# Kernel optimization log

Hardware: AMD Instinct MI355X
Metric: run time of the kernel (lower is better)

The kernel has to match this reference:

```python
import jax, jax.numpy as jnp
import numpy as np

D_MODEL = 1024
D_STATE = 32
D_CONV = 4
D_INNER = 2 * D_MODEL          # mamba default expand=2
DT_RANK = D_MODEL // 16        # 'auto' -> ceil(d_model/16)
BATCH, SEQ = 4, 2048
LN_EPS = 1e-5


def setup_inputs() -> dict:
    key = jax.random.key(0)
    ks = jax.random.split(key, 8)
    s = 0.02
    # S4D-real init for A_log, as in mamba_ssm
    A_log = jnp.log(jnp.tile(jnp.arange(1, D_STATE + 1, dtype=jnp.float32)[None, :], (D_INNER, 1)))
    return {
        "x": jax.random.normal(ks[0], (BATCH, SEQ, D_MODEL), jnp.float32),
        "in_proj_w": jax.random.normal(ks[1], (D_MODEL, 2 * D_INNER), jnp.float32) * s,
        "conv_w": jax.random.normal(ks[2], (D_INNER, D_CONV), jnp.float32) * s,
        "conv_b": jnp.zeros((D_INNER,), jnp.float32),
        "x_proj_w": jax.random.normal(ks[3], (D_INNER, DT_RANK + 2 * D_STATE), jnp.float32) * s,
        "dt_proj_w": jax.random.normal(ks[4], (DT_RANK, D_INNER), jnp.float32) * s,
        "dt_proj_b": jax.random.uniform(ks[5], (D_INNER,), jnp.float32, -4.0, -2.0),  # softplus -> small dt
        "A_log": A_log,
        "D": jnp.ones((D_INNER,), jnp.float32),
        "out_proj_w": jax.random.normal(ks[6], (D_INNER, D_MODEL), jnp.float32) * s,
        "ln_gamma": jnp.ones((D_MODEL,), jnp.float32),
        "ln_beta": jnp.zeros((D_MODEL,), jnp.float32),
    }


def reference(x, in_proj_w, conv_w, conv_b, x_proj_w, dt_proj_w, dt_proj_b,
              A_log, D, out_proj_w, ln_gamma, ln_beta):
    Bb, Ll, _ = x.shape
    # in_proj -> split into ssm branch (xi) and gate (z)
    xz = x @ in_proj_w                              # [B,L,2*Di]
    xi, z = jnp.split(xz, 2, axis=-1)               # each [B,L,Di]

    # causal depthwise conv1d (kernel D_CONV), left-padded, truncated to L
    xp = jnp.pad(xi, ((0, 0), (D_CONV - 1, 0), (0, 0)))
    xc = conv_b
    for k in range(D_CONV):
        xc = xc + xp[:, k:k + Ll, :] * conv_w[None, None, :, k]
    xi = jax.nn.silu(xc)                            # [B,L,Di]

    # x_proj -> dt, B, C
    dbc = xi @ x_proj_w                             # [B,L,dt_rank+2*S]
    dt = dbc[..., :DT_RANK]
    Bm = dbc[..., DT_RANK:DT_RANK + D_STATE]        # [B,L,S]
    Cm = dbc[..., DT_RANK + D_STATE:]               # [B,L,S]
    delta = jax.nn.softplus(dt @ dt_proj_w + dt_proj_b)  # [B,L,Di]

    A = -jnp.exp(A_log)                             # [Di,S]

    def step(h, inp):
        dl, bt, ct, ut = inp                        # [B,Di],[B,S],[B,S],[B,Di]
        dA = jnp.exp(dl[..., None] * A)             # [B,Di,S]
        h = dA * h + (dl * ut)[..., None] * bt[:, None, :]
        y = jnp.einsum('bds,bs->bd', h, ct)
        return h, y

    h0 = jnp.zeros((Bb, D_INNER, D_STATE), x.dtype)
    xs = (delta.transpose(1, 0, 2), Bm.transpose(1, 0, 2),
          Cm.transpose(1, 0, 2), xi.transpose(1, 0, 2))
    _, ys = jax.lax.scan(step, h0, xs)              # ys: [L,B,Di]

    y = ys.transpose(1, 0, 2) + xi * D              # skip term u*D
    y = y * jax.nn.silu(z)                          # gate
    out = y @ out_proj_w                            # [B,L,d_model]

    # LayerNorm(d_model)
    mu = out.mean(-1, keepdims=True)
    var = out.var(-1, keepdims=True)
    return (out - mu) / jnp.sqrt(var + LN_EPS) * ln_gamma + ln_beta
```

## Files before the change

### kernel.cpp

```cpp
#include <hip/hip_runtime.h>
#include <math.h>

#define D_MODEL 1024
#define D_STATE 32
#define D_CONV  4
#define D_INNER 2048
#define DT_RANK 64
#define BATCH   4
#define SEQ     2048
#define NTOK    (BATCH*SEQ)
#define DBC_N   (DT_RANK + 2*D_STATE)
#define NC      64
#define CL      (SEQ/NC)
#define KSPLIT  8
#define LOG2E   1.4426950408889634f

typedef unsigned short u16;
typedef short bf16x8 __attribute__((ext_vector_type(8)));
typedef float f32x4  __attribute__((ext_vector_type(4)));

__device__ __forceinline__ float bf2f(u16 u){
  return __uint_as_float(((unsigned)u) << 16);
}
__device__ __forceinline__ u16 f2bf(float f){
  unsigned u = __float_as_uint(f);
  return (u16)((u + 0x7fffu + ((u >> 16) & 1u)) >> 16);
}
__device__ __forceinline__ float sigmoidf_(float x){ return 1.f/(1.f+__expf(-x)); }
__device__ __forceinline__ float exp2_fast(float x){
  float r;
  asm("v_exp_f32 %0, %1" : "=v"(r) : "v"(x));
  return r;
}

typedef __attribute__((address_space(3))) void       lds_v;
typedef const __attribute__((address_space(1))) void gl_v;
#define GLOAD_LDS16(g, l) \
  __builtin_amdgcn_global_load_lds((gl_v*)(g), (lds_v*)(l), 16, 0, 0)

template<int MODE>
__global__ __launch_bounds__(256)
void mfma_gemm(int K,
               const u16* __restrict__ A, int lda,
               const u16* __restrict__ B, int ldb,
               void* __restrict__ C1, int ldc,
               u16*  __restrict__ C2)
{
  __shared__ u16 As[128*32];
  __shared__ u16 Bs[128*32];
  const int tid  = threadIdx.x;
  const int lane = tid & 63;
  const int wave = tid >> 6;
  const int wm = (wave>>1)*64, wn = (wave&1)*64;
  const int m0 = blockIdx.y*128, n0 = blockIdx.x*128;

  const int srow = tid >> 2;
  const int scs  = (((tid & 3) ^ ((srow >> 1) & 3)) * 8);

  const u16* Ag = A + (size_t)(m0 + srow)*lda + scs;
  const u16* Bg = B + (size_t)(n0 + srow)*ldb + scs;

  const int fr = lane & 15;
  const int fq = lane >> 4;
  const int sx = (fr >> 1) & 3;
  const int rdoff = ((fq ^ sx) * 8);
  f32x4 acc[4][4] = {};

  u16* as0 = &As[tid*8];
  u16* as1 = &As[2048 + tid*8];
  u16* bs0 = &Bs[tid*8];
  u16* bs1 = &Bs[2048 + tid*8];

  for (int k0=0; k0<K; k0+=32){
    GLOAD_LDS16(Ag + k0,                    as0);
    GLOAD_LDS16(Ag + (size_t)64*lda + k0,   as1);
    GLOAD_LDS16(Bg + k0,                    bs0);
    GLOAD_LDS16(Bg + (size_t)64*ldb + k0,   bs1);
    __syncthreads();

    bf16x8 af[4], bfr[4];
    #pragma unroll
    for (int i=0;i<4;i++){
      af[i]  = *(const bf16x8*)&As[(wm + i*16 + fr)*32 + rdoff];
      bfr[i] = *(const bf16x8*)&Bs[(wn + i*16 + fr)*32 + rdoff];
    }
    #pragma unroll
    for (int mi=0;mi<4;mi++)
      #pragma unroll
      for (int ni=0;ni<4;ni++)
        acc[mi][ni] = __builtin_amdgcn_mfma_f32_16x16x32_bf16(
            af[mi], bfr[ni], acc[mi][ni], 0, 0, 0);
    __syncthreads();
  }

  const bool second = (MODE==2) && (n0 >= D_INNER);
  #pragma unroll
  for (int mi=0;mi<4;mi++){
    #pragma unroll
    for (int ni=0;ni<4;ni++){
      int col = n0 + wn + ni*16 + fr;
      #pragma unroll
      for (int r=0;r<4;r++){
        int row = m0 + wm + mi*16 + fq*4 + r;
        float v = acc[mi][ni][r];
        if (MODE==0)      ((float*)C1)[(size_t)row*ldc + col] = v;
        else {
          if (second) C2[(size_t)row*D_INNER + (col - D_INNER)] = f2bf(v);
          else        ((float*)C1)[(size_t)row*D_INNER + col] = v;
        }
      }
    }
  }
}

__global__ __launch_bounds__(256)
void cvt_f32_bf16(const float* __restrict__ in, u16* __restrict__ out)
{
  size_t i = (size_t)blockIdx.x*256 + threadIdx.x;
  float4 v = ((const float4*)in)[i];
  ushort4 o;
  o.x=f2bf(v.x); o.y=f2bf(v.y); o.z=f2bf(v.z); o.w=f2bf(v.w);
  ((ushort4*)out)[i] = o;
}

__global__ __launch_bounds__(256)
void transpose_cvt(const float* __restrict__ in, u16* __restrict__ out,
                   int R, int C)
{
  __shared__ float tile[64][65];
  const int bc = blockIdx.x*64, br = blockIdx.y*64;
  const int tx = threadIdx.x & 63, ty = threadIdx.x >> 6;
  #pragma unroll
  for (int i=0;i<16;i++){
    int r = ty + i*4;
    tile[r][tx] = in[(size_t)(br+r)*C + bc+tx];
  }
  __syncthreads();
  #pragma unroll
  for (int i=0;i<16;i++){
    int r = ty + i*4;
    out[(size_t)(bc+r)*R + br+tx] = f2bf(tile[tx][r]);
  }
}

template<int BM,int BN,int BK,int TM,int TN,int EPI>
__global__ __launch_bounds__((BM/TM)*(BN/TN))
void sgemm(int K,
           const float* __restrict__ A,int lda,
           const float* __restrict__ B,int ldb,
           float* __restrict__ C,int ldc,
           const float* __restrict__ bias)
{
  __shared__ float As[BK][BM];
  __shared__ float Bs[BK][BN];
  const int tid  = threadIdx.x;
  const int brow = blockIdx.y, bcol = blockIdx.x;
  const int tcol = tid % (BN/TN);
  const int trow = tid / (BN/TN);

  const float* Ag = A + (size_t)brow*BM*lda;
  const float* Bg = B + (size_t)bcol*BN;

  const int arow = tid / (BK/4);
  const int acol = (tid % (BK/4))*4;
  const int brw  = tid / (BN/4);
  const int bcv  = (tid % (BN/4))*4;

  float acc[TM][TN] = {};

  for (int k0=0; k0<K; k0+=BK){
    float4 av = *(const float4*)(Ag + (size_t)arow*lda + k0 + acol);
    float4 bv = *(const float4*)(Bg + (size_t)(k0+brw)*ldb + bcv);
    __syncthreads();
    As[acol+0][arow]=av.x; As[acol+1][arow]=av.y;
    As[acol+2][arow]=av.z; As[acol+3][arow]=av.w;
    *(float4*)&Bs[brw][bcv] = bv;
    __syncthreads();
    #pragma unroll
    for (int kk=0;kk<BK;kk++){
      float ra[TM], rb[TN];
      #pragma unroll
      for (int m=0;m<TM;m++) ra[m]=As[kk][trow*TM+m];
      #pragma unroll
      for (int n=0;n<TN;n++) rb[n]=Bs[kk][tcol*TN+n];
      #pragma unroll
      for (int m=0;m<TM;m++)
        #pragma unroll
        for (int n=0;n<TN;n++)
          acc[m][n] += ra[m]*rb[n];
    }
  }

  #pragma unroll
  for (int m=0;m<TM;m++){
    int row = brow*BM + trow*TM + m;
    #pragma unroll
    for (int n=0;n<TN;n++){
      int col = bcol*BN + tcol*TN + n;
      float v = acc[m][n];
      if (EPI==1){
        v += bias[col];
        v = (v > 20.f) ? v : log1pf(__expf(v));
      }
      C[(size_t)row*ldc + col] = v;
    }
  }
}

__global__ __launch_bounds__(256)
void sgemm_pk(int K,
              const float* __restrict__ A,int lda,
              const float* __restrict__ B,int ldb,
              float* __restrict__ part)
{
  const int BM=64, BN=64, BK=16, TM=4, TN=4;
  __shared__ float As[BK][BM];
  __shared__ float Bs[BK][BN];
  const int tid  = threadIdx.x;
  const int brow = blockIdx.y, bcol = blockIdx.x, kz = blockIdx.z;
  const int Kc   = K / KSPLIT;
  const int tcol = tid % (BN/TN);
  const int trow = tid / (BN/TN);

  const float* Ag = A + (size_t)brow*BM*lda + (size_t)kz*Kc;
  const float* Bg = B + (size_t)kz*Kc*ldb + (size_t)bcol*BN;

  const int arow = tid / (BK/4);
  const int acol = (tid % (BK/4))*4;
  const int brw  = tid / (BN/4);
  const int bcv  = (tid % (BN/4))*4;

  float acc[TM][TN] = {};

  for (int k0=0; k0<Kc; k0+=BK){
    float4 av = *(const float4*)(Ag + (size_t)arow*lda + k0 + acol);
    float4 bv = *(const float4*)(Bg + (size_t)(k0+brw)*ldb + bcv);
    __syncthreads();
    As[acol+0][arow]=av.x; As[acol+1][arow]=av.y;
    As[acol+2][arow]=av.z; As[acol+3][arow]=av.w;
    *(float4*)&Bs[brw][bcv] = bv;
    __syncthreads();
    #pragma unroll
    for (int kk=0;kk<BK;kk++){
      float ra[TM], rb[TN];
      #pragma unroll
      for (int m=0;m<TM;m++) ra[m]=As[kk][trow*TM+m];
      #pragma unroll
      for (int n=0;n<TN;n++) rb[n]=Bs[kk][tcol*TN+n];
      #pragma unroll
      for (int m=0;m<TM;m++)
        #pragma unroll
        for (int n=0;n<TN;n++)
          acc[m][n] += ra[m]*rb[n];
    }
  }

  float* P = part + (size_t)kz*NTOK*DBC_N;
  #pragma unroll
  for (int m=0;m<TM;m++){
    int row = brow*BM + trow*TM + m;
    #pragma unroll
    for (int n=0;n<TN;n++){
      int col = bcol*BN + tcol*TN + n;
      P[(size_t)row*DBC_N + col] = acc[m][n];
    }
  }
}

__global__ __launch_bounds__(256)
void reduce_pk(const float* __restrict__ part, float* __restrict__ dbc)
{
  size_t i = (size_t)blockIdx.x*256 + threadIdx.x;
  const size_t stride4 = (size_t)NTOK*DBC_N/4;
  float4 s = ((const float4*)part)[i];
  #pragma unroll
  for (int z=1; z<KSPLIT; ++z){
    float4 v = ((const float4*)part)[z*stride4 + i];
    s.x+=v.x; s.y+=v.y; s.z+=v.z; s.w+=v.w;
  }
  ((float4*)dbc)[i] = s;
}

__global__ __launch_bounds__(256)
void conv_silu_kernel(const float* __restrict__ xi_raw,
                      const float* __restrict__ conv_w,
                      const float* __restrict__ conv_b,
                      float* __restrict__ xi_post)
{
  size_t idx = (size_t)blockIdx.x*256 + threadIdx.x;
  int d = (int)(idx % D_INNER);
  size_t bt = idx / D_INNER;
  int t = (int)(bt % SEQ);
  size_t b = bt / SEQ;
  const float* xi = xi_raw + b*(size_t)SEQ*D_INNER;
  float accv = conv_b[d];
  #pragma unroll
  for (int k=0;k<D_CONV;k++){
    int tt = t + k - (D_CONV-1);
    if (tt >= 0) accv += xi[(size_t)tt*D_INNER + d] * conv_w[d*D_CONV + k];
  }
  xi_post[idx] = accv * sigmoidf_(accv);
}

__global__ __launch_bounds__(256)
void scan_part1(const float* __restrict__ dbc,
                const float* __restrict__ delta,
                const float* __restrict__ u,
                const float* __restrict__ A_log,
                float* __restrict__ q,
                float* __restrict__ sumdl_buf)
{
  const int ndg  = D_INNER/256;
  const int dgrp = blockIdx.x % ndg;
  const int c    = (blockIdx.x / ndg) % NC;
  const int b    =  blockIdx.x / (ndg*NC);
  const int d    = dgrp*256 + threadIdx.x;

  const float* Ap = A_log + (size_t)d*D_STATE;
  const float base = -__expf(Ap[0]) * LOG2E;
  bool fastp = true;
  #pragma unroll
  for (int s=1; s<D_STATE; ++s){
    float a2 = -__expf(Ap[s]) * LOG2E;
    float ideal = base * (float)(s+1);
    fastp = fastp && (fabsf(a2 - ideal) <= 1e-4f*fabsf(ideal));
  }

  const size_t tok0 = (size_t)b*SEQ + (size_t)c*CL;
  const float* dptr = delta + tok0*D_INNER + d;
  const float* uptr = u     + tok0*D_INNER + d;
  const float* dbcp = dbc   + tok0*DBC_N;

  float h[D_STATE] = {};
  float sumdl = 0.f;

  if (fastp){
    for (int t=0; t<CL; ++t){
      float dl = dptr[(size_t)t*D_INNER];
      float uu = uptr[(size_t)t*D_INNER];
      sumdl += dl;
      float w  = dl*uu;
      float E  = exp2_fast(dl*base);
      float E2 = E*E, E3 = E2*E, E4 = E2*E2;
      float P  = 1.f;
      const float4* B4 = (const float4*)(dbcp + (size_t)t*DBC_N + DT_RANK);
      #pragma unroll
      for (int g=0; g<8; ++g){
        float4 Bv = B4[g];
        float m0 = P*E, m1 = P*E2, m2 = P*E3, m3 = P*E4;
        h[4*g+0] = m0*h[4*g+0] + w*Bv.x;
        h[4*g+1] = m1*h[4*g+1] + w*Bv.y;
        h[4*g+2] = m2*h[4*g+2] + w*Bv.z;
        h[4*g+3] = m3*h[4*g+3] + w*Bv.w;
        P = m3;
      }
    }
  } else {
    float A2[D_STATE];
    #pragma unroll
    for (int g=0; g<8; ++g){
      float4 al = *(const float4*)(Ap + 4*g);
      A2[4*g+0] = -__expf(al.x)*LOG2E; A2[4*g+1] = -__expf(al.y)*LOG2E;
      A2[4*g+2] = -__expf(al.z)*LOG2E; A2[4*g+3] = -__expf(al.w)*LOG2E;
    }
    for (int t=0; t<CL; ++t){
      float dl = dptr[(size_t)t*D_INNER];
      float uu = uptr[(size_t)t*D_INNER];
      sumdl += dl;
      float w = dl*uu;
      const float4* B4 = (const float4*)(dbcp + (size_t)t*DBC_N + DT_RANK);
      #pragma unroll
      for (int g=0; g<8; ++g){
        float4 Bv = B4[g];
        h[4*g+0] = exp2_fast(dl*A2[4*g+0])*h[4*g+0] + w*Bv.x;
        h[4*g+1] = exp2_fast(dl*A2[4*g+1])*h[4*g+1] + w*Bv.y;
        h[4*g+2] = exp2_fast(dl*A2[4*g+2])*h[4*g+2] + w*Bv.z;
        h[4*g+3] = exp2_fast(dl*A2[4*g+3])*h[4*g+3] + w*Bv.w;
      }
    }
  }

  float* qp = q + (((size_t)b*NC + c)*D_INNER + d)*D_STATE;
  #pragma unroll
  for (int g=0; g<8; ++g)
    ((float4*)qp)[g] = make_float4(h[4*g+0],h[4*g+1],h[4*g+2],h[4*g+3]);
  sumdl_buf[((size_t)b*NC + c)*D_INNER + d] = sumdl;
}

__global__ __launch_bounds__(256)
void scan_combine(float* __restrict__ q,
                  const float* __restrict__ sumdl_buf,
                  const float* __restrict__ A_log)
{
  size_t idx = (size_t)blockIdx.x*256 + threadIdx.x;
  int s = (int)(idx % D_STATE);
  size_t dd = idx / D_STATE;
  int d = (int)(dd % D_INNER);
  int b = (int)(dd / D_INNER);

  const float As2 = -__expf(A_log[(size_t)d*D_STATE + s]) * LOG2E;
  float H = 0.f;
  for (int c=0; c<NC; ++c){
    size_t off = (((size_t)b*NC + c)*D_INNER + d)*D_STATE + s;
    float tmp = q[off];
    q[off] = H;
    H = exp2_fast(As2 * sumdl_buf[((size_t)b*NC + c)*D_INNER + d]) * H + tmp;
  }
}

__global__ __launch_bounds__(256)
void scan_part2(const float* __restrict__ dbc,
                const float* __restrict__ delta,
                const float* __restrict__ u,
                u16*         __restrict__ zy,
                const float* __restrict__ q,
                const float* __restrict__ A_log,
                const float* __restrict__ Dp)
{
  const int ndg  = D_INNER/256;
  const int dgrp = blockIdx.x % ndg;
  const int c    = (blockIdx.x / ndg) % NC;
  const int b    =  blockIdx.x / (ndg*NC);
  const int d    = dgrp*256 + threadIdx.x;

  const float* Ap = A_log + (size_t)d*D_STATE;
  const float base = -__expf(Ap[0]) * LOG2E;
  bool fastp = true;
  #pragma unroll
  for (int s=1; s<D_STATE; ++s){
    float a2 = -__expf(Ap[s]) * LOG2E;
    float ideal = base * (float)(s+1);
    fastp = fastp && (fabsf(a2 - ideal) <= 1e-4f*fabsf(ideal));
  }

  float h[D_STATE];
  const float* qp = q + (((size_t)b*NC + c)*D_INNER + d)*D_STATE;
  #pragma unroll
  for (int g=0; g<8; ++g){
    float4 hv = ((const float4*)qp)[g];
    h[4*g+0]=hv.x; h[4*g+1]=hv.y; h[4*g+2]=hv.z; h[4*g+3]=hv.w;
  }
  const float Dd = Dp[d];

  const size_t tok0 = (size_t)b*SEQ + (size_t)c*CL;
  const float* dptr = delta + tok0*D_INNER + d;
  const float* uptr = u     + tok0*D_INNER + d;
  u16*         zp   = zy    + tok0*D_INNER + d;
  const float* dbcp = dbc   + tok0*DBC_N;

  if (fastp){
    for (int t=0; t<CL; ++t){
      float dl = dptr[(size_t)t*D_INNER];
      float uu = uptr[(size_t)t*D_INNER];
      float zz = bf2f(zp[(size_t)t*D_INNER]);
      float w  = dl*uu;
      float E  = exp2_fast(dl*base);
      float E2 = E*E, E3 = E2*E, E4 = E2*E2;
      float P  = 1.f;
      const float4* B4 = (const float4*)(dbcp + (size_t)t*DBC_N + DT_RANK);
      const float4* C4 = B4 + 8;
      float y = 0.f;
      #pragma unroll
      for (int g=0; g<8; ++g){
        float4 Bv = B4[g];
        float4 Cv = C4[g];
        float m0 = P*E, m1 = P*E2, m2 = P*E3, m3 = P*E4;
        h[4*g+0] = m0*h[4*g+0] + w*Bv.x;  y += h[4*g+0]*Cv.x;
        h[4*g+1] = m1*h[4*g+1] + w*Bv.y;  y += h[4*g+1]*Cv.y;
        h[4*g+2] = m2*h[4*g+2] + w*Bv.z;  y += h[4*g+2]*Cv.z;
        h[4*g+3] = m3*h[4*g+3] + w*Bv.w;  y += h[4*g+3]*Cv.w;
        P = m3;
      }
      zp[(size_t)t*D_INNER] = f2bf((y + uu*Dd) * (zz * sigmoidf_(zz)));
    }
  } else {
    float A2[D_STATE];
    #pragma unroll
    for (int g=0; g<8; ++g){
      float4 al = *(const float4*)(Ap + 4*g);
      A2[4*g+0] = -__expf(al.x)*LOG2E; A2[4*g+1] = -__expf(al.y)*LOG2E;
      A2[4*g+2] = -__expf(al.z)*LOG2E; A2[4*g+3] = -__expf(al.w)*LOG2E;
    }
    for (int t=0; t<CL; ++t){
      float dl = dptr[(size_t)t*D_INNER];
      float uu = uptr[(size_t)t*D_INNER];
      float zz = bf2f(zp[(size_t)t*D_INNER]);
      float w  = dl*uu;
      const float4* B4 = (const float4*)(dbcp + (size_t)t*DBC_N + DT_RANK);
      const float4* C4 = B4 + 8;
      float y = 0.f;
      #pragma unroll
      for (int g=0; g<8; ++g){
        float4 Bv = B4[g];
        float4 Cv = C4[g];
        h[4*g+0] = exp2_fast(dl*A2[4*g+0])*h[4*g+0] + w*Bv.x;  y += h[4*g+0]*Cv.x;
        h[4*g+1] = exp2_fast(dl*A2[4*g+1])*h[4*g+1] + w*Bv.y;  y += h[4*g+1]*Cv.y;
        h[4*g+2] = exp2_fast(dl*A2[4*g+2])*h[4*g+2] + w*Bv.z;  y += h[4*g+2]*Cv.z;
        h[4*g+3] = exp2_fast(dl*A2[4*g+3])*h[4*g+3] + w*Bv.w;  y += h[4*g+3]*Cv.w;
      }
      zp[(size_t)t*D_INNER] = f2bf((y + uu*Dd) * (zz * sigmoidf_(zz)));
    }
  }
}

__global__ __launch_bounds__(256)
void ln_kernel(const float* __restrict__ in,
               float* __restrict__ out,
               const float* __restrict__ gamma,
               const float* __restrict__ beta)
{
  const int row = blockIdx.x;
  const float* p = in + (size_t)row*D_MODEL;
  float* q = out + (size_t)row*D_MODEL;
  float v[4]; float s=0.f, ss=0.f;
  #pragma unroll
  for (int i=0;i<4;i++){
    float x = p[i*256 + threadIdx.x];
    v[i]=x; s+=x; ss+=x*x;
  }
  #pragma unroll
  for (int off=32; off; off>>=1){
    s  += __shfl_xor(s,  off, 64);
    ss += __shfl_xor(ss, off, 64);
  }
  __shared__ float sw[4], ssw[4];
  const int wid = threadIdx.x >> 6;
  if ((threadIdx.x & 63) == 0){ sw[wid]=s; ssw[wid]=ss; }
  __syncthreads();
  s  = sw[0]+sw[1]+sw[2]+sw[3];
  ss = ssw[0]+ssw[1]+ssw[2]+ssw[3];
  const float mu  = s * (1.f/D_MODEL);
  const float var = ss * (1.f/D_MODEL) - mu*mu;
  const float inv = rsqrtf(var + 1e-5f);
  #pragma unroll
  for (int i=0;i<4;i++){
    int col = i*256 + threadIdx.x;
    q[col] = (v[i]-mu)*inv*gamma[col] + beta[col];
  }
}

extern "C" void kernel_launch(void* const* d_in, const int* in_sizes, int n_in,
                              void* d_out, int out_size, void* d_ws, size_t ws_size,
                              hipStream_t stream)
{
  const float* x          = (const float*)d_in[0];
  const float* in_proj_w  = (const float*)d_in[1];
  const float* conv_w     = (const float*)d_in[2];
  const float* conv_b     = (const float*)d_in[3];
  const float* x_proj_w   = (const float*)d_in[4];
  const float* dt_proj_w  = (const float*)d_in[5];
  const float* dt_proj_b  = (const float*)d_in[6];
  const float* A_log      = (const float*)d_in[7];
  const float* Dp         = (const float*)d_in[8];
  const float* out_proj_w = (const float*)d_in[9];
  const float* ln_gamma   = (const float*)d_in[10];
  const float* ln_beta    = (const float*)d_in[11];
  float* out = (float*)d_out;

  char* ws = (char*)d_ws;
  float* xi_raw  = (float*)(ws + 0);
  float* pkpart  = (float*)(ws + 0);
  float* deltab  = (float*)(ws + 0);
  float* preln   = (float*)(ws + 0);
  float* xi_post = (float*)(ws + (size_t) 67108864);
  u16*   zybuf   = (u16*)  (ws + (size_t)134217728);
  u16*   x_bf    = (u16*)  (ws + (size_t)167772160);
  float* dbc     = (float*)(ws + (size_t)167772160);
  float* qbuf    = (float*)(ws + (size_t)171966464);
  float* sumdl   = (float*)(ws + (size_t)239075328);
  u16*   w_inT   = (u16*)  (ws + (size_t)241172480);
  u16*   w_outT  = (u16*)  (ws + (size_t)249561088);

  cvt_f32_bf16<<<(NTOK*(size_t)D_MODEL)/1024, 256, 0, stream>>>(x, x_bf);
  { dim3 g(4096/64, 1024/64); transpose_cvt<<<g,256,0,stream>>>(in_proj_w,  w_inT,  1024, 4096); }
  { dim3 g(1024/64, 2048/64); transpose_cvt<<<g,256,0,stream>>>(out_proj_w, w_outT, 2048, 1024); }

  {
    dim3 grid(2*D_INNER/128, NTOK/128);
    mfma_gemm<2><<<grid,256,0,stream>>>(D_MODEL,
        x_bf, D_MODEL, w_inT, D_MODEL, xi_raw, 0, zybuf);
  }
  conv_silu_kernel<<<(NTOK*(size_t)D_INNER)/256,256,0,stream>>>(xi_raw, conv_w, conv_b, xi_post);

  {
    dim3 grid(DBC_N/64, NTOK/64, KSPLIT);
    sgemm_pk<<<grid,256,0,stream>>>(D_INNER,
        xi_post,D_INNER, x_proj_w,DBC_N, pkpart);
    reduce_pk<<<(NTOK*(size_t)DBC_N)/1024,256,0,stream>>>(pkpart, dbc);
  }
  {
    dim3 grid(D_INNER/64, NTOK/64);
    sgemm<64,64,16,4,4,1><<<grid,256,0,stream>>>(DT_RANK,
        dbc,DBC_N, dt_proj_w,D_INNER, deltab,D_INNER, dt_proj_b);
  }
  {
    dim3 grid1((D_INNER/256)*NC*BATCH);
    scan_part1<<<grid1,256,0,stream>>>(dbc, deltab, xi_post, A_log, qbuf, sumdl);
    scan_combine<<<(BATCH*(size_t)D_INNER*D_STATE)/256,256,0,stream>>>(qbuf, sumdl, A_log);
    scan_part2<<<grid1,256,0,stream>>>(dbc, deltab, xi_post, zybuf, qbuf, A_log, Dp);
  }
  {
    dim3 grid(D_MODEL/128, NTOK/128);
    mfma_gemm<0><<<grid,256,0,stream>>>(D_INNER,
        zybuf, D_INNER, w_outT, D_INNER, preln, D_MODEL, nullptr);
  }
  ln_kernel<<<NTOK,256,0,stream>>>(preln, out, ln_gamma, ln_beta);
}
```

Measured before the change: 664.7 us.

## Run x_proj and dt_proj GEMMs on bf16 MFMA kernel instead of fp32 sgemm

Removes the fp32 SIMT sgemm kernels for the x_proj (split-K) and dt_proj GEMMs. Both now go through the existing bf16 MFMA GEMM via two new epilogue modes: split-K partial output, and bias plus softplus. The conv kernel also writes a bf16 copy of the post-SiLU activations. The split-K reduction also writes a bf16 copy of the dt slice, and both weight matrices are transposed and converted to bf16. This trades an extra activation write and some bf16 rounding in the delta/B/C path for much faster matrix-core compute.

After: 623.0 us. 6.3% less time.

```diff
diff --git a/kernel.cpp b/kernel.cpp
--- a/kernel.cpp
+++ b/kernel.cpp
@@ -44,7 +44,8 @@
                const u16* __restrict__ A, int lda,
                const u16* __restrict__ B, int ldb,
                void* __restrict__ C1, int ldc,
-               u16*  __restrict__ C2)
+               u16*  __restrict__ C2,
+               const float* __restrict__ bias)
 {
   __shared__ u16 As[128*32];
   __shared__ u16 Bs[128*32];
@@ -53,12 +54,13 @@
   const int wave = tid >> 6;
   const int wm = (wave>>1)*64, wn = (wave&1)*64;
   const int m0 = blockIdx.y*128, n0 = blockIdx.x*128;
+  const size_t koff = (MODE==3) ? (size_t)blockIdx.z*K : 0;
 
   const int srow = tid >> 2;
   const int scs  = (((tid & 3) ^ ((srow >> 1) & 3)) * 8);
 
-  const u16* Ag = A + (size_t)(m0 + srow)*lda + scs;
-  const u16* Bg = B + (size_t)(n0 + srow)*ldb + scs;
+  const u16* Ag = A + (size_t)(m0 + srow)*lda + scs + koff;
+  const u16* Bg = B + (size_t)(n0 + srow)*ldb + scs + koff;
 
   const int fr = lane & 15;
   const int fq = lane >> 4;
@@ -92,6 +94,9 @@
             af[mi], bfr[ni], acc[mi][ni], 0, 0, 0);
     __syncthreads();
   }
+
+  float* Cf = (float*)C1;
+  if (MODE==3) Cf += (size_t)blockIdx.z*((size_t)NTOK*DBC_N);
 
   const bool second = (MODE==2) && (n0 >= D_INNER);
   #pragma unroll
@@ -103,10 +108,15 @@
       for (int r=0;r<4;r++){
         int row = m0 + wm + mi*16 + fq*4 + r;
         float v = acc[mi][ni][r];
-        if (MODE==0)      ((float*)C1)[(size_t)row*ldc + col] = v;
-        else {
+        if (MODE==0 || MODE==3){
+          Cf[(size_t)row*ldc + col] = v;
+        } else if (MODE==4){
+          v += bias[col];
+          v = (v > 20.f) ? v : log1pf(__expf(v));
+          Cf[(size_t)row*ldc + col] = v;
+        } else {
           if (second) C2[(size_t)row*D_INNER + (col - D_INNER)] = f2bf(v);
-          else        ((float*)C1)[(size_t)row*D_INNER + col] = v;
+          else        Cf[(size_t)row*D_INNER + col] = v;
         }
       }
     }
@@ -143,132 +153,9 @@
   }
 }
 
-template<int BM,int BN,int BK,int TM,int TN,int EPI>
-__global__ __launch_bounds__((BM/TM)*(BN/TN))
-void sgemm(int K,
-           const float* __restrict__ A,int lda,
-           const float* __restrict__ B,int ldb,
-           float* __restrict__ C,int ldc,
-           const float* __restrict__ bias)
-{
-  __shared__ float As[BK][BM];
-  __shared__ float Bs[BK][BN];
-  const int tid  = threadIdx.x;
-  const int brow = blockIdx.y, bcol = blockIdx.x;
-  const int tcol = tid % (BN/TN);
-  const int trow = tid / (BN/TN);
-
-  const float* Ag = A + (size_t)brow*BM*lda;
-  const float* Bg = B + (size_t)bcol*BN;
-
-  const int arow = tid / (BK/4);
-  const int acol = (tid % (BK/4))*4;
-  const int brw  = tid / (BN/4);
-  const int bcv  = (tid % (BN/4))*4;
-
-  float acc[TM][TN] = {};
-
-  for (int k0=0; k0<K; k0+=BK){
-    float4 av = *(const float4*)(Ag + (size_t)arow*lda + k0 + acol);
-    float4 bv = *(const float4*)(Bg + (size_t)(k0+brw)*ldb + bcv);
-    __syncthreads();
-    As[acol+0][arow]=av.x; As[acol+1][arow]=av.y;
-    As[acol+2][arow]=av.z; As[acol+3][arow]=av.w;
-    *(float4*)&Bs[brw][bcv] = bv;
-    __syncthreads();
-    #pragma unroll
-    for (int kk=0;kk<BK;kk++){
-      float ra[TM], rb[TN];
-      #pragma unroll
-      for (int m=0;m<TM;m++) ra[m]=As[kk][trow*TM+m];
-      #pragma unroll
-      for (int n=0;n<TN;n++) rb[n]=Bs[kk][tcol*TN+n];
-      #pragma unroll
-      for (int m=0;m<TM;m++)
-        #pragma unroll
-        for (int n=0;n<TN;n++)
-          acc[m][n] += ra[m]*rb[n];
-    }
-  }
-
-  #pragma unroll
-  for (int m=0;m<TM;m++){
-    int row = brow*BM + trow*TM + m;
-    #pragma unroll
-    for (int n=0;n<TN;n++){
-      int col = bcol*BN + tcol*TN + n;
-      float v = acc[m][n];
-      if (EPI==1){
-        v += bias[col];
-        v = (v > 20.f) ? v : log1pf(__expf(v));
-      }
-      C[(size_t)row*ldc + col] = v;
-    }
-  }
-}
-
-__global__ __launch_bounds__(256)
-void sgemm_pk(int K,
-              const float* __restrict__ A,int lda,
-              const float* __restrict__ B,int ldb,
-              float* __restrict__ part)
-{
-  const int BM=64, BN=64, BK=16, TM=4, TN=4;
-  __shared__ float As[BK][BM];
-  __shared__ float Bs[BK][BN];
-  const int tid  = threadIdx.x;
-  const int brow = blockIdx.y, bcol = blockIdx.x, kz = blockIdx.z;
-  const int Kc   = K / KSPLIT;
-  const int tcol = tid % (BN/TN);
-  const int trow = tid / (BN/TN);
-
-  const float* Ag = A + (size_t)brow*BM*lda + (size_t)kz*Kc;
-  const float* Bg = B + (size_t)kz*Kc*ldb + (size_t)bcol*BN;
-
-  const int arow = tid / (BK/4);
-  const int acol = (tid % (BK/4))*4;
-  const int brw  = tid / (BN/4);
-  const int bcv  = (tid % (BN/4))*4;
-
-  float acc[TM][TN] = {};
-
-  for (int k0=0; k0<Kc; k0+=BK){
-    float4 av = *(const float4*)(Ag + (size_t)arow*lda + k0 + acol);
-    float4 bv = *(const float4*)(Bg + (size_t)(k0+brw)*ldb + bcv);
-    __syncthreads();
-    As[acol+0][arow]=av.x; As[acol+1][arow]=av.y;
-    As[acol+2][arow]=av.z; As[acol+3][arow]=av.w;
-    *(float4*)&Bs[brw][bcv] = bv;
-    __syncthreads();
-    #pragma unroll
-    for (int kk=0;kk<BK;kk++){
-      float ra[TM], rb[TN];
-      #pragma unroll
-      for (int m=0;m<TM;m++) ra[m]=As[kk][trow*TM+m];
-      #pragma unroll
-      for (int n=0;n<TN;n++) rb[n]=Bs[kk][tcol*TN+n];
-      #pragma unroll
-      for (int m=0;m<TM;m++)
-        #pragma unroll
-        for (int n=0;n<TN;n++)
-          acc[m][n] += ra[m]*rb[n];
-    }
-  }
-
-  float* P = part + (size_t)kz*NTOK*DBC_N;
-  #pragma unroll
-  for (int m=0;m<TM;m++){
-    int row = brow*BM + trow*TM + m;
-    #pragma unroll
-    for (int n=0;n<TN;n++){
-      int col = bcol*BN + tcol*TN + n;
-      P[(size_t)row*DBC_N + col] = acc[m][n];
-    }
-  }
-}
-
-__global__ __launch_bounds__(256)
-void reduce_pk(const float* __restrict__ part, float* __restrict__ dbc)
+__global__ __launch_bounds__(256)
+void reduce_pk(const float* __restrict__ part, float* __restrict__ dbc,
+               u16* __restrict__ dtbf)
 {
   size_t i = (size_t)blockIdx.x*256 + threadIdx.x;
   const size_t stride4 = (size_t)NTOK*DBC_N/4;
@@ -279,13 +166,21 @@
     s.x+=v.x; s.y+=v.y; s.z+=v.z; s.w+=v.w;
   }
   ((float4*)dbc)[i] = s;
+  int j = (int)(i & 31);
+  if (j < 16){
+    size_t row = i >> 5;
+    ushort4 o;
+    o.x=f2bf(s.x); o.y=f2bf(s.y); o.z=f2bf(s.z); o.w=f2bf(s.w);
+    *(ushort4*)(dtbf + row*DT_RANK + 4*j) = o;
+  }
 }
 
 __global__ __launch_bounds__(256)
 void conv_silu_kernel(const float* __restrict__ xi_raw,
                       const float* __restrict__ conv_w,
                       const float* __restrict__ conv_b,
-                      float* __restrict__ xi_post)
+                      float* __restrict__ xi_post,
+                      u16*   __restrict__ xi_bf)
 {
   size_t idx = (size_t)blockIdx.x*256 + threadIdx.x;
   int d = (int)(idx % D_INNER);
@@ -299,7 +194,9 @@
     int tt = t + k - (D_CONV-1);
     if (tt >= 0) accv += xi[(size_t)tt*D_INNER + d] * conv_w[d*D_CONV + k];
   }
-  xi_post[idx] = accv * sigmoidf_(accv);
+  float res = accv * sigmoidf_(accv);
+  xi_post[idx] = res;
+  xi_bf[idx]   = f2bf(res);
 }
 
 __global__ __launch_bounds__(256)
@@ -566,32 +463,39 @@
   u16*   zybuf   = (u16*)  (ws + (size_t)134217728);
   u16*   x_bf    = (u16*)  (ws + (size_t)167772160);
   float* dbc     = (float*)(ws + (size_t)167772160);
+  u16*   xi_bf   = (u16*)  (ws + (size_t)171966464);
   float* qbuf    = (float*)(ws + (size_t)171966464);
   float* sumdl   = (float*)(ws + (size_t)239075328);
   u16*   w_inT   = (u16*)  (ws + (size_t)241172480);
   u16*   w_outT  = (u16*)  (ws + (size_t)249561088);
+  u16*   x_projT = (u16*)  (ws + (size_t)253755392);
+  u16*   dt_projT= (u16*)  (ws + (size_t)254279680);
+  u16*   dtbf    = (u16*)  (ws + (size_t)254803968);
 
   cvt_f32_bf16<<<(NTOK*(size_t)D_MODEL)/1024, 256, 0, stream>>>(x, x_bf);
   { dim3 g(4096/64, 1024/64); transpose_cvt<<<g,256,0,stream>>>(in_proj_w,  w_inT,  1024, 4096); }
   { dim3 g(1024/64, 2048/64); transpose_cvt<<<g,256,0,stream>>>(out_proj_w, w_outT, 2048, 1024); }
+  { dim3 g( 128/64, 2048/64); transpose_cvt<<<g,256,0,stream>>>(x_proj_w,   x_projT, 2048, 128); }
+  { dim3 g(2048/64,   64/64); transpose_cvt<<<g,256,0,stream>>>(dt_proj_w,  dt_projT,  64, 2048); }
 
   {
     dim3 grid(2*D_INNER/128, NTOK/128);
     mfma_gemm<2><<<grid,256,0,stream>>>(D_MODEL,
-        x_bf, D_MODEL, w_inT, D_MODEL, xi_raw, 0, zybuf);
-  }
-  conv_silu_kernel<<<(NTOK*(size_t)D_INNER)/256,256,0,stream>>>(xi_raw, conv_w, conv_b, xi_post);
+        x_bf, D_MODEL, w_inT, D_MODEL, xi_raw, 0, zybuf, nullptr);
+  }
+  conv_silu_kernel<<<(NTOK*(size_t)D_INNER)/256,256,0,stream>>>(
+      xi_raw, conv_w, conv_b, xi_post, xi_bf);
 
   {
-    dim3 grid(DBC_N/64, NTOK/64, KSPLIT);
-    sgemm_pk<<<grid,256,0,stream>>>(D_INNER,
-        xi_post,D_INNER, x_proj_w,DBC_N, pkpart);
-    reduce_pk<<<(NTOK*(size_t)DBC_N)/1024,256,0,stream>>>(pkpart, dbc);
+    dim3 grid(DBC_N/128, NTOK/128, KSPLIT);
+    mfma_gemm<3><<<grid,256,0,stream>>>(D_INNER/KSPLIT,
+        xi_bf, D_INNER, x_projT, D_INNER, pkpart, DBC_N, nullptr, nullptr);
+    reduce_pk<<<(NTOK*(size_t)DBC_N)/1024,256,0,stream>>>(pkpart, dbc, dtbf);
   }
   {
-    dim3 grid(D_INNER/64, NTOK/64);
-    sgemm<64,64,16,4,4,1><<<grid,256,0,stream>>>(DT_RANK,
-        dbc,DBC_N, dt_proj_w,D_INNER, deltab,D_INNER, dt_proj_b);
+    dim3 grid(D_INNER/128, NTOK/128);
+    mfma_gemm<4><<<grid,256,0,stream>>>(DT_RANK,
+        dtbf, DT_RANK, dt_projT, DT_RANK, deltab, D_INNER, nullptr, dt_proj_b);
   }
   {
     dim3 grid1((D_INNER/256)*NC*BATCH);
@@ -602,7 +506,7 @@
   {
     dim3 grid(D_MODEL/128, NTOK/128);
     mfma_gemm<0><<<grid,256,0,stream>>>(D_INNER,
-        zybuf, D_INNER, w_outT, D_INNER, preln, D_MODEL, nullptr);
+        zybuf, D_INNER, w_outT, D_INNER, preln, D_MODEL, nullptr, nullptr);
   }
   ln_kernel<<<NTOK,256,0,stream>>>(preln, out, ln_gamma, ln_beta);
 }
```
